# Kernel optimization log

Measured on AMD Instinct MI355X. Metric: run time of the kernel, lower is better.

The kernel has to match this reference:

```python
import jax, jax.numpy as jnp
import numpy as np

LN_EPS = 1e-5

def _layernorm(x, g, b):
    mu = jnp.mean(x, axis=-1, keepdims=True)
    var = jnp.var(x, axis=-1, keepdims=True)
    return (x - mu) / jnp.sqrt(var + LN_EPS) * g + b

def setup_inputs() -> dict:
    key = jax.random.key(0)
    ks = jax.random.split(key, 12)
    N, D_WSI, D_OMIC, D, DH = 50000, 1024, 1577, 256, 128
    def rn(k, shape, s=0.02):
        return jax.random.normal(k, shape, jnp.float32) * s
    return {
        'wsi': jax.random.normal(ks[0], (N, D_WSI), jnp.float32),
        'x_omic': jax.random.normal(ks[1], (D_OMIC,), jnp.float32),
        # SNNOmics: Linear(1577,256)+ELU, Linear(256,256)+ELU (AlphaDropout=eval identity)
        'W1': rn(ks[2], (D_OMIC, 256)), 'b1': jnp.zeros((256,), jnp.float32),
        'W2': rn(ks[3], (256, 256)), 'b2': jnp.zeros((256,), jnp.float32),
        # wsi projection Linear(1024,256)
        'Wp': rn(ks[4], (D_WSI, D)), 'bp': jnp.zeros((D,), jnp.float32),
        # MMAttentionLayer pre-norm (dim=256)
        'ln1_g': jnp.ones((D,), jnp.float32), 'ln1_b': jnp.zeros((D,), jnp.float32),
        # to_qkv: Linear(256, 3*heads*dim_head) = Linear(256, 384), no bias (heads=1, dim_head=128)
        'Wqkv': rn(ks[5], (D, 3 * DH)),
        # FeedForward(dim=128, mult=1): LN + Linear(128,128)+GELU+Linear(128,128) (no residual)
        'ln2_g': jnp.ones((DH,), jnp.float32), 'ln2_b': jnp.zeros((DH,), jnp.float32),
        'Wf1': rn(ks[6], (DH, DH)), 'bf1': jnp.zeros((DH,), jnp.float32),
        'Wf2': rn(ks[7], (DH, DH)), 'bf2': jnp.zeros((DH,), jnp.float32),
        # final LayerNorm(128)
        'ln3_g': jnp.ones((DH,), jnp.float32), 'ln3_b': jnp.zeros((DH,), jnp.float32),
        # to_logits: Linear(256,64)+ReLU+Linear(64,4)
        'Wl1': rn(ks[8], (2 * DH, 64)), 'bl1': jnp.zeros((64,), jnp.float32),
        'Wl2': rn(ks[9], (64, 4)), 'bl2': jnp.zeros((4,), jnp.float32),
    }

def reference(wsi, x_omic, W1, b1, W2, b2, Wp, bp, ln1_g, ln1_b, Wqkv,
              ln2_g, ln2_b, Wf1, bf1, Wf2, bf2, ln3_g, ln3_b, Wl1, bl1, Wl2, bl2):
    M = 1            # num_pathways
    DH = 128         # dim_head (heads=1)
    scale = DH ** -0.5
    # SNN omics encoder -> one pathway token [1, 256]
    h = jax.nn.elu(x_omic @ W1 + b1)
    h = jax.nn.elu(h @ W2 + b2)
    h_omic = h[None, :]                              # [1, 256]
    # WSI projection -> histology tokens [N, 256]
    wsi_embed = wsi @ Wp + bp                        # [N, 256]
    tokens = jnp.concatenate([h_omic, wsi_embed], axis=0)   # [1+N, 256]
    # MMAttentionLayer: pre-norm then asymmetric pathway/histology attention
    xn = _layernorm(tokens, ln1_g, ln1_b)
    qkv = xn @ Wqkv                                  # [1+N, 384]
    q, k, v = jnp.split(qkv, 3, axis=-1)             # each [1+N, 128]
    q = q * scale
    q_p, q_h = q[:M], q[M:]                          # [1,128], [N,128]
    k_p, k_h = k[:M], k[M:]
    # cross attention: histology -> pathways (rows of length M=1)
    cross_attn_hist = q_h @ k_p.T                    # [N, 1]
    cross_attn_hist = jax.nn.softmax(cross_attn_hist, axis=-1)
    # pathway row attends to [pathways | histology]
    attn_p = q_p @ k_p.T                             # [1, 1]
    cross_attn_p = q_p @ k_h.T                       # [1, N]
    attn_ph = jax.nn.softmax(jnp.concatenate([attn_p, cross_attn_p], axis=-1), axis=-1)  # [1, 1+N]
    out_p = attn_ph @ v                              # [1, 128]
    out_h = cross_attn_hist @ v[:M]                  # [N, 128]
    out = jnp.concatenate([out_p, out_h], axis=0)    # [1+N, 128] (residual=False: no conv)
    # FeedForward (no residual add in original) + LayerNorm
    mm = _layernorm(out, ln2_g, ln2_b)
    mm = jax.nn.gelu(mm @ Wf1 + bf1, approximate=False) @ Wf2 + bf2
    mm = _layernorm(mm, ln3_g, ln3_b)                # [1+N, 128]
    paths_embed = jnp.mean(mm[:M], axis=0)           # [128]
    wsi_embed_post = jnp.mean(mm[M:], axis=0)        # [128]
    embedding = jnp.concatenate([paths_embed, wsi_embed_post])[None, :]  # [1, 256]
    logits = jax.nn.relu(embedding @ Wl1 + bl1) @ Wl2 + bl2              # [1, 4]
    prob = jax.nn.softmax(logits, axis=-1)
    return logits, prob
```

## Files before the change

### kernel.cpp

```cpp
#include <hip/hip_runtime.h>
#include <hip/hip_bf16.h>
#include <math.h>

#define LN_EPS 1e-5f

typedef unsigned short ushortT;
typedef short bf16x8 __attribute__((ext_vector_type(8)));
typedef float f32x4 __attribute__((ext_vector_type(4)));

#define WS_QP   0
#define WS_V0   128
#define WS_S0   256
#define WS_H1P  512
#define WS_PART 4608
#define PART_STRIDE 260
#define PART_M 256
#define PART_L 257
#define WS_Z    107000
#define WS_GP   109000
#define GP_STRIDE 260
#define NCOMB   32
#define WS_WPT  131072

__device__ __forceinline__ float elu1(float x){ return x > 0.f ? x : expm1f(x); }
__device__ __forceinline__ unsigned pk2(float lo, float hi){
  union { __hip_bfloat162 h; unsigned u; } cv;
  cv.h = __float22bfloat162_rn(make_float2(lo, hi));
  return cv.u;
}
__device__ __forceinline__ void dma16(const void* g, void* l) {
  __builtin_amdgcn_global_load_lds(
      (const __attribute__((address_space(1))) unsigned int*)g,
      (__attribute__((address_space(3))) unsigned int*)l, 16, 0, 0);
}
template<int N> __device__ __forceinline__ void vwait() {
  asm volatile("s_waitcnt vmcnt(%0)" :: "i"(N) : "memory");
}
__device__ __forceinline__ void lwait0() {
  asm volatile("s_waitcnt lgkmcnt(0)" ::: "memory");
}
__device__ __forceinline__ void sbar()   { __builtin_amdgcn_s_barrier(); }
__device__ __forceinline__ void schedb() { __builtin_amdgcn_sched_barrier(0); }

__global__ __launch_bounds__(256) void k_setup(
    const float* __restrict__ Wp,
    const float* __restrict__ x, const float* __restrict__ W1, int d_omic,
    ushortT* __restrict__ wpt, float* __restrict__ ws)
{
  int bb = blockIdx.x, t = threadIdx.x;
  if (bb < 32) {
    int kc = bb, m = t, sw = (m >> 1) & 3;
    #pragma unroll
    for (int c = 0; c < 4; ++c) {
      float v[8];
      #pragma unroll
      for (int e = 0; e < 8; ++e) v[e] = Wp[(size_t)(kc * 32 + c * 8 + e) * 256 + m];
      uint4 w = make_uint4(pk2(v[0], v[1]), pk2(v[2], v[3]), pk2(v[4], v[5]), pk2(v[6], v[7]));
      *(uint4*)&wpt[kc * 8192 + m * 32 + ((c ^ sw) * 8)] = w;
    }
  } else {
    int g = bb - 32;
    int i0 = g * 99, i1 = min(i0 + 99, d_omic);
    __shared__ float xs[112];
    for (int i = i0 + t; i < i1; i += 256) xs[i - i0] = x[i];
    __syncthreads();
    float s = 0.f;
    for (int i = i0; i < i1; i++) s = fmaf(xs[i - i0], W1[(size_t)i * 256 + t], s);
    ws[WS_H1P + g * 256 + t] = s;
  }
}

__global__ __launch_bounds__(256) void k_omic(
    const float* __restrict__ b1,
    const float* __restrict__ W2, const float* __restrict__ b2,
    const float* __restrict__ Wqkv,
    const float* __restrict__ ln1_g, const float* __restrict__ ln1_b,
    float* __restrict__ ws)
{
  __shared__ float h1[256];
  __shared__ float xn0[256];
  __shared__ float qs[128], ks[128];
  __shared__ float red[8];
  int tid = threadIdx.x, lane = tid & 63, wave = tid >> 6;

  float s = b1[tid];
  for (int g = 0; g < 16; g++) s += ws[WS_H1P + g * 256 + tid];
  h1[tid] = elu1(s);
  __syncthreads();

  s = b2[tid];
  for (int i = 0; i < 256; i++) s = fmaf(h1[i], W2[i * 256 + tid], s);
  float t0 = elu1(s);

  float ps = t0, pq = t0 * t0;
  for (int m = 1; m < 64; m <<= 1) { ps += __shfl_xor(ps, m); pq += __shfl_xor(pq, m); }
  if (lane == 0) { red[wave] = ps; red[4 + wave] = pq; }
  __syncthreads();
  float mu = (red[0] + red[1] + red[2] + red[3]) * (1.f / 256.f);
  float var = (red[4] + red[5] + red[6] + red[7]) * (1.f / 256.f) - mu * mu;
  float xn = (t0 - mu) * rsqrtf(var + LN_EPS) * ln1_g[tid] + ln1_b[tid];
  xn0[tid] = xn;
  __syncthreads();

  float a = 0.f;
  for (int j = 0; j < 256; j++) a = fmaf(xn0[j], Wqkv[j * 384 + tid], a);
  if (tid < 128) { float q = a * 0.088388347648318447f; qs[tid] = q; ws[WS_QP + tid] = q; }
  else           { ks[tid - 128] = a; }
  if (tid < 128) {
    float av = 0.f;
    for (int j = 0; j < 256; j++) av = fmaf(xn0[j], Wqkv[j * 384 + 256 + tid], av);
    ws[WS_V0 + tid] = av;
  }
  __syncthreads();
  float p = (tid < 128) ? qs[tid] * ks[tid] : 0.f;
  for (int m = 1; m < 64; m <<= 1) p += __shfl_xor(p, m);
  if (lane == 0) red[wave] = p;
  __syncthreads();
  if (tid == 0) ws[WS_S0] = red[0] + red[1] + red[2] + red[3];

  float zv = 0.f;
  #pragma unroll 4
  for (int d = 0; d < 128; d += 4) {
    float4 q4 = *(const float4*)&qs[d];
    const float* wr_ = &Wqkv[tid * 384 + 128 + d];
    zv = fmaf(q4.x, wr_[0], zv);
    zv = fmaf(q4.y, wr_[1], zv);
    zv = fmaf(q4.z, wr_[2], zv);
    zv = fmaf(q4.w, wr_[3], zv);
  }
  ws[WS_Z + tid] = zv;
}

__global__ __launch_bounds__(512, 4) void k_main(
    const float* __restrict__ wsi, int N,
    const ushortT* __restrict__ wpt,
    const float* __restrict__ bp,
    const float* __restrict__ ln1_g, const float* __restrict__ ln1_b,
    float* __restrict__ ws)
{
  __shared__ __align__(16) char U[81920];

  const int tid = threadIdx.x;
  const int lane = tid & 63, wv = tid >> 6;
  const int l15 = lane & 15, lh = lane >> 4;
  const int cg = wv & 3, rg = wv >> 2;
  const int b = blockIdx.x, r0 = b * 128;

  int wsiSrc[2];
  #pragma unroll
  for (int i = 0; i < 2; ++i) {
    int rowL = 16 * wv + 8 * i + (lane >> 3);
    int gr = r0 + rowL; gr = (gr < N) ? gr : (N - 1);
    wsiSrc[i] = gr * 1024 + (((lane & 7) ^ (lane >> 3)) << 2);
  }
  int wptSrc[2];
  #pragma unroll
  for (int j = 0; j < 2; ++j) wptSrc[j] = (32 * wv + 16 * j) * 32 + lane * 8;

  const unsigned afslot = (unsigned)((lh ^ ((l15 >> 1) & 3)) << 4);
  const unsigned bs0 = (unsigned)(((2 * lh)     ^ (l15 & 7)) << 4);
  const unsigned bs1 = (unsigned)(((2 * lh + 1) ^ (l15 & 7)) << 4);

  const f32x4 z4i = {0.f, 0.f, 0.f, 0.f};
  f32x4 acc[4][4];
  #pragma unroll
  for (int mt = 0; mt < 4; ++mt)
    #pragma unroll
    for (int nt = 0; nt < 4; ++nt) acc[mt][nt] = z4i;

  auto stageWsi = [&](int kc, int slot) {
    char* ds = U + slot * 16384 + wv * 2048;
    #pragma unroll
    for (int i = 0; i < 2; ++i) dma16(wsi + wsiSrc[i] + kc * 32, ds + i * 1024);
  };
  auto stageWpt = [&](int kc, int slot) {
    char* dw = U + 49152 + slot * 16384 + wv * 2048;
    #pragma unroll
    for (int j = 0; j < 2; ++j) dma16(wpt + wptSrc[j] + kc * 8192, dw + j * 1024);
  };

  stageWsi(0, 0); stageWpt(0, 0);
  stageWsi(1, 1); stageWpt(1, 1);
  stageWsi(2, 2);
  for (int s = 0; s < 32; ++s) {
    if (s < 30) vwait<6>(); else if (s == 30) vwait<4>(); else vwait<0>();
    sbar(); schedb();
    {
      const char* Ws = U + (s % 3) * 16384;
      const char* Wf = U + 49152 + (s & 1) * 16384;
      bf16x8 af[4], bfr[4];
      #pragma unroll
      for (int mt = 0; mt < 4; ++mt)
        af[mt] = *(const bf16x8*)(Wf + (64 * cg + 16 * mt + l15) * 64 + afslot);
      #pragma unroll
      for (int nt = 0; nt < 4; ++nt) {
        const char* p = Ws + (64 * rg + 16 * nt + l15) * 128;
        uint4 ua = *(const uint4*)(p + bs0);
        uint4 ub = *(const uint4*)(p + bs1);
        union { unsigned u[4]; bf16x8 v; } cv;
        cv.u[0] = pk2(__uint_as_float(ua.x), __uint_as_float(ua.y));
        cv.u[1] = pk2(__uint_as_float(ua.z), __uint_as_float(ua.w));
        cv.u[2] = pk2(__uint_as_float(ub.x), __uint_as_float(ub.y));
        cv.u[3] = pk2(__uint_as_float(ub.z), __uint_as_float(ub.w));
        bfr[nt] = cv.v;
      }
      #pragma unroll
      for (int mt = 0; mt < 4; ++mt)
        #pragma unroll
        for (int nt = 0; nt < 4; ++nt)
          acc[mt][nt] = __builtin_amdgcn_mfma_f32_16x16x32_bf16(af[mt], bfr[nt], acc[mt][nt], 0, 0, 0);
    }
    sbar(); schedb();
    if (s < 30) stageWpt(s + 2, s & 1);
    if (s < 29) stageWsi(s + 3, s % 3);
  }

  float* red = (float*)(U + 65536);
  float4 bp4[4], g4[4], b4[4];
  #pragma unroll
  for (int mt = 0; mt < 4; ++mt) {
    int m0 = 64 * cg + 16 * mt + 4 * lh;
    bp4[mt] = *(const float4*)&bp[m0];
    g4[mt]  = *(const float4*)&ln1_g[m0];
    b4[mt]  = *(const float4*)&ln1_b[m0];
  }
  float ps[4], pq[4];
  #pragma unroll
  for (int nt = 0; nt < 4; ++nt) { ps[nt] = 0.f; pq[nt] = 0.f; }
  #pragma unroll
  for (int mt = 0; mt < 4; ++mt) {
    const float bb4[4] = {bp4[mt].x, bp4[mt].y, bp4[mt].z, bp4[mt].w};
    #pragma unroll
    for (int nt = 0; nt < 4; ++nt)
      #pragma unroll
      for (int r = 0; r < 4; ++r) {
        float v = acc[mt][nt][r] + bb4[r];
        acc[mt][nt][r] = v;
        ps[nt] += v; pq[nt] += v * v;
      }
  }
  #pragma unroll
  for (int nt = 0; nt < 4; ++nt) {
    ps[nt] += __shfl_xor(ps[nt], 16); pq[nt] += __shfl_xor(pq[nt], 16);
    ps[nt] += __shfl_xor(ps[nt], 32); pq[nt] += __shfl_xor(pq[nt], 32);
  }
  if (lh == 0) {
    #pragma unroll
    for (int nt = 0; nt < 4; ++nt) {
      int row = 64 * rg + 16 * nt + l15;
      *(float2*)&red[row * 8 + cg * 2] = make_float2(ps[nt], pq[nt]);
    }
  }
  lwait0(); sbar(); schedb();
  float mu[4], rstd[4];
  #pragma unroll
  for (int nt = 0; nt < 4; ++nt) {
    int row = 64 * rg + 16 * nt + l15;
    float s_ = 0.f, q_ = 0.f;
    #pragma unroll
    for (int c = 0; c < 4; ++c) { s_ += red[row * 8 + c * 2]; q_ += red[row * 8 + c * 2 + 1]; }
    float m_ = s_ * (1.f / 256.f);
    float v_ = q_ * (1.f / 256.f) - m_ * m_;
    mu[nt] = m_; rstd[nt] = rsqrtf(v_ + LN_EPS);
  }

  #pragma unroll
  for (int mt = 0; mt < 4; ++mt)
    #pragma unroll
    for (int nt = 0; nt < 4; ++nt) {
      acc[mt][nt][0] = (acc[mt][nt][0] - mu[nt]) * rstd[nt] * g4[mt].x + b4[mt].x;
      acc[mt][nt][1] = (acc[mt][nt][1] - mu[nt]) * rstd[nt] * g4[mt].y + b4[mt].y;
      acc[mt][nt][2] = (acc[mt][nt][2] - mu[nt]) * rstd[nt] * g4[mt].z + b4[mt].z;
      acc[mt][nt][3] = (acc[mt][nt][3] - mu[nt]) * rstd[nt] * g4[mt].w + b4[mt].w;
    }

  float* sred = (float*)U;
  float* aux  = (float*)(U + 2048);
  float* wts  = (float*)(U + 2112);
  float* vred = (float*)(U + 3072);
  float* part = ws + WS_PART + (size_t)b * PART_STRIDE;

  {
    float4 zf[4];
    #pragma unroll
    for (int mt = 0; mt < 4; ++mt)
      zf[mt] = *(const float4*)&ws[WS_Z + 64 * cg + 16 * mt + 4 * lh];
    float sp[4];
    #pragma unroll
    for (int nt = 0; nt < 4; ++nt) {
      float s_ = 0.f;
      #pragma unroll
      for (int mt = 0; mt < 4; ++mt) {
        s_ = fmaf(zf[mt].x, acc[mt][nt][0], s_);
        s_ = fmaf(zf[mt].y, acc[mt][nt][1], s_);
        s_ = fmaf(zf[mt].z, acc[mt][nt][2], s_);
        s_ = fmaf(zf[mt].w, acc[mt][nt][3], s_);
      }
      sp[nt] = s_;
    }
    #pragma unroll
    for (int nt = 0; nt < 4; ++nt) {
      sp[nt] += __shfl_xor(sp[nt], 16);
      sp[nt] += __shfl_xor(sp[nt], 32);
    }
    if (lh == 0) {
      #pragma unroll
      for (int nt = 0; nt < 4; ++nt) sred[cg * 128 + 64 * rg + 16 * nt + l15] = sp[nt];
    }
  }
  lwait0(); sbar(); schedb();

  float sv = -INFINITY, ev = 0.f;
  if (tid < 128) {
    sv = sred[tid] + sred[128 + tid] + sred[256 + tid] + sred[384 + tid];
    if (r0 + tid >= N) sv = -INFINITY;
  }
  float mb = sv;
  #pragma unroll
  for (int m = 1; m < 64; m <<= 1) mb = fmaxf(mb, __shfl_xor(mb, m));
  if (tid < 128 && lane == 0) aux[tid >> 6] = mb;
  lwait0(); sbar(); schedb();
  float M2 = fmaxf(aux[0], aux[1]);
  if (tid < 128) { ev = (r0 + tid < N) ? expf(sv - M2) : 0.f; wts[tid] = ev; }
  float lsum = ev;
  #pragma unroll
  for (int m = 1; m < 64; m <<= 1) lsum += __shfl_xor(lsum, m);
  if (tid < 128 && lane == 0) aux[2 + (tid >> 6)] = lsum;
  lwait0(); sbar(); schedb();
  if (tid == 0) { part[PART_M] = M2; part[PART_L] = aux[2] + aux[3]; }

  {
    float wr[4];
    #pragma unroll
    for (int nt = 0; nt < 4; ++nt) wr[nt] = wts[64 * rg + 16 * nt + l15];
    #pragma unroll
    for (int mt = 0; mt < 4; ++mt) {
      float vs0 = 0.f, vs1 = 0.f, vs2 = 0.f, vs3 = 0.f;
      #pragma unroll
      for (int nt = 0; nt < 4; ++nt) {
        vs0 = fmaf(wr[nt], acc[mt][nt][0], vs0);
        vs1 = fmaf(wr[nt], acc[mt][nt][1], vs1);
        vs2 = fmaf(wr[nt], acc[mt][nt][2], vs2);
        vs3 = fmaf(wr[nt], acc[mt][nt][3], vs3);
      }
      #pragma unroll
      for (int m = 1; m < 16; m <<= 1) {
        vs0 += __shfl_xor(vs0, m); vs1 += __shfl_xor(vs1, m);
        vs2 += __shfl_xor(vs2, m); vs3 += __shfl_xor(vs3, m);
      }
      if (l15 == 0)
        *(float4*)&vred[256 * rg + 64 * cg + 16 * mt + 4 * lh] =
            make_float4(vs0, vs1, vs2, vs3);
    }
  }
  lwait0(); sbar(); schedb();
  if (tid < 256) part[tid] = vred[tid] + vred[256 + tid];
}

__global__ __launch_bounds__(256) void k_fin1(float* __restrict__ ws, int NB, int chunk)
{
  int g = blockIdx.x, col = threadIdx.x;
  int c0 = g * chunk, c1 = min(c0 + chunk, NB);
  const float* part = ws + WS_PART;
  float mg = -INFINITY;
  for (int bb = c0; bb < c1; ++bb)
    mg = fmaxf(mg, part[(size_t)bb * PART_STRIDE + PART_M]);
  float a = 0.f, lg = 0.f;
  for (int bb = c0; bb < c1; ++bb) {
    float w = expf(part[(size_t)bb * PART_STRIDE + PART_M] - mg);
    a  = fmaf(part[(size_t)bb * PART_STRIDE + col], w, a);
    lg = fmaf(part[(size_t)bb * PART_STRIDE + PART_L], w, lg);
  }
  ws[WS_GP + g * GP_STRIDE + col] = a;
  if (col == 0) {
    ws[WS_GP + g * GP_STRIDE + PART_M] = mg;
    ws[WS_GP + g * GP_STRIDE + PART_L] = lg;
  }
}

__global__ __launch_bounds__(256) void k_final(
    const float* __restrict__ ws, const float* __restrict__ Wqkv,
    const float* __restrict__ Wf1, const float* __restrict__ bf1,
    const float* __restrict__ Wf2, const float* __restrict__ bf2,
    const float* __restrict__ ln2_g, const float* __restrict__ ln2_b,
    const float* __restrict__ ln3_g, const float* __restrict__ ln3_b,
    const float* __restrict__ Wl1, const float* __restrict__ bl1,
    const float* __restrict__ Wl2, const float* __restrict__ bl2,
    float* __restrict__ out)
{
  __shared__ float rowb[2][128];
  __shared__ float mmb[2][128];
  __shared__ float red[8];
  __shared__ float emb[256];
  __shared__ float abuf[64];
  __shared__ float lbuf[4];
  __shared__ float wg[NCOMB];
  __shared__ float MLs[2];
  __shared__ float Ybuf[256];
  int tid = threadIdx.x, lane = tid & 63, wave = tid >> 6;
  float s0 = ws[WS_S0];

  if (tid == 0) {
    float M = s0;
    for (int g = 0; g < NCOMB; ++g) M = fmaxf(M, ws[WS_GP + g * GP_STRIDE + PART_M]);
    float L = expf(s0 - M);
    for (int g = 0; g < NCOMB; ++g)
      L = fmaf(ws[WS_GP + g * GP_STRIDE + PART_L], expf(ws[WS_GP + g * GP_STRIDE + PART_M] - M), L);
    MLs[0] = M; MLs[1] = L;
  }
  __syncthreads();
  float M = MLs[0], L = MLs[1];
  if (tid < NCOMB) wg[tid] = expf(ws[WS_GP + tid * GP_STRIDE + PART_M] - M);
  __syncthreads();

  {
    float y = 0.f;
    #pragma unroll
    for (int g = 0; g < NCOMB; ++g) y = fmaf(ws[WS_GP + g * GP_STRIDE + tid], wg[g], y);
    Ybuf[tid] = y;
  }
  __syncthreads();

  if (tid < 128) {
    float v0 = ws[WS_V0 + tid];
    float a = v0 * expf(s0 - M);
    for (int c = 0; c < 256; ++c)
      a = fmaf(Ybuf[c], Wqkv[c * 384 + 256 + tid], a);
    rowb[0][tid] = a / L;
    rowb[1][tid] = v0;
  }
  __syncthreads();

  int row = tid >> 7, k = tid & 127;
  float x = rowb[row][k];
  float ps = x, pq = x * x;
  for (int m = 1; m < 64; m <<= 1) { ps += __shfl_xor(ps, m); pq += __shfl_xor(pq, m); }
  __syncthreads();
  if (lane == 0) { red[wave] = ps; red[4 + wave] = pq; }
  __syncthreads();
  {
    float sum = red[row * 2] + red[row * 2 + 1];
    float sq  = red[4 + row * 2] + red[4 + row * 2 + 1];
    float mu = sum * (1.f / 128.f);
    float var = sq * (1.f / 128.f) - mu * mu;
    x = (x - mu) * rsqrtf(var + LN_EPS) * ln2_g[k] + ln2_b[k];
  }
  mmb[row][k] = x;
  __syncthreads();
  float t1 = bf1[k];
  for (int j = 0; j < 128; j++) t1 = fmaf(mmb[row][j], Wf1[j * 128 + k], t1);
  float gg = t1 * 0.5f * (1.f + erff(t1 * 0.70710678118654752f));
  __syncthreads();
  rowb[row][k] = gg;
  __syncthreads();
  float t2 = bf2[k];
  for (int j = 0; j < 128; j++) t2 = fmaf(rowb[row][j], Wf2[j * 128 + k], t2);
  ps = t2; pq = t2 * t2;
  for (int m = 1; m < 64; m <<= 1) { ps += __shfl_xor(ps, m); pq += __shfl_xor(pq, m); }
  __syncthreads();
  if (lane == 0) { red[wave] = ps; red[4 + wave] = pq; }
  __syncthreads();
  {
    float sum = red[row * 2] + red[row * 2 + 1];
    float sq  = red[4 + row * 2] + red[4 + row * 2 + 1];
    float mu = sum * (1.f / 128.f);
    float var = sq * (1.f / 128.f) - mu * mu;
    t2 = (t2 - mu) * rsqrtf(var + LN_EPS) * ln3_g[k] + ln3_b[k];
  }
  emb[row * 128 + k] = t2;
  __syncthreads();
  if (tid < 64) {
    float a = bl1[tid];
    for (int j = 0; j < 256; j++) a = fmaf(emb[j], Wl1[j * 64 + tid], a);
    abuf[tid] = fmaxf(a, 0.f);
  }
  __syncthreads();
  if (tid < 4) {
    float lg = bl2[tid];
    for (int j = 0; j < 64; j++) lg = fmaf(abuf[j], Wl2[j * 4 + tid], lg);
    lbuf[tid] = lg;
  }
  __syncthreads();
  if (tid < 4) {
    float m4 = fmaxf(fmaxf(lbuf[0], lbuf[1]), fmaxf(lbuf[2], lbuf[3]));
    float e0 = expf(lbuf[0] - m4), e1 = expf(lbuf[1] - m4);
    float e2 = expf(lbuf[2] - m4), e3 = expf(lbuf[3] - m4);
    float ssum = e0 + e1 + e2 + e3;
    out[tid] = lbuf[tid];
    out[4 + tid] = expf(lbuf[tid] - m4) / ssum;
  }
}

extern "C" void kernel_launch(void* const* d_in, const int* in_sizes, int n_in,
                              void* d_out, int out_size, void* d_ws, size_t ws_size,
                              hipStream_t stream) {
  const float* wsi    = (const float*)d_in[0];
  const float* x_omic = (const float*)d_in[1];
  const float* W1     = (const float*)d_in[2];
  const float* b1     = (const float*)d_in[3];
  const float* W2     = (const float*)d_in[4];
  const float* b2     = (const float*)d_in[5];
  const float* Wp     = (const float*)d_in[6];
  const float* bp     = (const float*)d_in[7];
  const float* ln1_g  = (const float*)d_in[8];
  const float* ln1_b  = (const float*)d_in[9];
  const float* Wqkv   = (const float*)d_in[10];
  const float* ln2_g  = (const float*)d_in[11];
  const float* ln2_b  = (const float*)d_in[12];
  const float* Wf1    = (const float*)d_in[13];
  const float* bf1    = (const float*)d_in[14];
  const float* Wf2    = (const float*)d_in[15];
  const float* bf2    = (const float*)d_in[16];
  const float* ln3_g  = (const float*)d_in[17];
  const float* ln3_b  = (const float*)d_in[18];
  const float* Wl1    = (const float*)d_in[19];
  const float* bl1    = (const float*)d_in[20];
  const float* Wl2    = (const float*)d_in[21];
  const float* bl2    = (const float*)d_in[22];
  float* ws   = (float*)d_ws;
  float* outp = (float*)d_out;
  ushortT* wpt = (ushortT*)(ws + WS_WPT);

  int N = in_sizes[0] / 1024;
  int d_omic = in_sizes[1];
  int NB = (N + 127) / 128;
  int chunk = (NB + NCOMB - 1) / NCOMB;

  k_setup<<<48, 256, 0, stream>>>(Wp, x_omic, W1, d_omic, wpt, ws);
  k_omic<<<1, 256, 0, stream>>>(b1, W2, b2, Wqkv, ln1_g, ln1_b, ws);
  k_main<<<NB, 512, 0, stream>>>(wsi, N, wpt, bp, ln1_g, ln1_b, ws);
  k_fin1<<<NCOMB, 256, 0, stream>>>(ws, NB, chunk);
  k_final<<<1, 256, 0, stream>>>(ws, Wqkv, Wf1, bf1, Wf2, bf2, ln2_g, ln2_b,
                                 ln3_g, ln3_b, Wl1, bl1, Wl2, bl2, outp);
}
```

Measured before the change: 141.7 us.

## Halve k_main row tile and load weight fragments directly from global

The main projection kernel now processes 64 wsi rows per block instead of 128, which doubles the block count. The bf16 weight tile is no longer staged through LDS; each wave loads its A fragments from global memory (L2) into registers, double-buffered across pairs of K slices. This cuts shared memory from 80KB to 24KB and raises the launch-bounds occupancy target. In exchange the weights are reused less per block, global/L2 weight traffic rises, and more partial results have to be combined, so the partial buffer is moved to a larger workspace offset.

```diff
diff --git a/kernel.cpp b/kernel.cpp
--- a/kernel.cpp
+++ b/kernel.cpp
@@ -12,15 +12,15 @@
 #define WS_V0   128
 #define WS_S0   256
 #define WS_H1P  512
-#define WS_PART 4608
-#define PART_STRIDE 260
-#define PART_M 256
-#define PART_L 257
 #define WS_Z    107000
 #define WS_GP   109000
 #define GP_STRIDE 260
 #define NCOMB   32
 #define WS_WPT  131072
+#define WS_PART 262144
+#define PART_STRIDE 260
+#define PART_M 256
+#define PART_L 257
 
 __device__ __forceinline__ float elu1(float x){ return x > 0.f ? x : expm1f(x); }
 __device__ __forceinline__ unsigned pk2(float lo, float hi){
@@ -131,91 +131,95 @@
   ws[WS_Z + tid] = zv;
 }
 
-__global__ __launch_bounds__(512, 4) void k_main(
+__global__ __launch_bounds__(512, 6) void k_main(
     const float* __restrict__ wsi, int N,
     const ushortT* __restrict__ wpt,
     const float* __restrict__ bp,
     const float* __restrict__ ln1_g, const float* __restrict__ ln1_b,
     float* __restrict__ ws)
 {
-  __shared__ __align__(16) char U[81920];
+  __shared__ __align__(16) char U[24576];
 
   const int tid = threadIdx.x;
   const int lane = tid & 63, wv = tid >> 6;
   const int l15 = lane & 15, lh = lane >> 4;
   const int cg = wv & 3, rg = wv >> 2;
-  const int b = blockIdx.x, r0 = b * 128;
-
-  int wsiSrc[2];
-  #pragma unroll
-  for (int i = 0; i < 2; ++i) {
-    int rowL = 16 * wv + 8 * i + (lane >> 3);
+  const int b = blockIdx.x, r0 = b * 64;
+
+  int wsiSrc;
+  {
+    int rowL = 8 * wv + (lane >> 3);
     int gr = r0 + rowL; gr = (gr < N) ? gr : (N - 1);
-    wsiSrc[i] = gr * 1024 + (((lane & 7) ^ (lane >> 3)) << 2);
-  }
-  int wptSrc[2];
-  #pragma unroll
-  for (int j = 0; j < 2; ++j) wptSrc[j] = (32 * wv + 16 * j) * 32 + lane * 8;
-
-  const unsigned afslot = (unsigned)((lh ^ ((l15 >> 1) & 3)) << 4);
+    wsiSrc = gr * 1024 + (((lane & 7) ^ (lane >> 3)) << 2);
+  }
+  int afBase[4];
+  #pragma unroll
+  for (int mt = 0; mt < 4; ++mt) {
+    int m = 64 * cg + 16 * mt + l15;
+    afBase[mt] = m * 32 + ((lh ^ ((m >> 1) & 3)) << 3);
+  }
+
   const unsigned bs0 = (unsigned)(((2 * lh)     ^ (l15 & 7)) << 4);
   const unsigned bs1 = (unsigned)(((2 * lh + 1) ^ (l15 & 7)) << 4);
 
   const f32x4 z4i = {0.f, 0.f, 0.f, 0.f};
-  f32x4 acc[4][4];
+  f32x4 acc[4][2];
   #pragma unroll
   for (int mt = 0; mt < 4; ++mt)
     #pragma unroll
-    for (int nt = 0; nt < 4; ++nt) acc[mt][nt] = z4i;
+    for (int nt = 0; nt < 2; ++nt) acc[mt][nt] = z4i;
 
   auto stageWsi = [&](int kc, int slot) {
-    char* ds = U + slot * 16384 + wv * 2048;
-    #pragma unroll
-    for (int i = 0; i < 2; ++i) dma16(wsi + wsiSrc[i] + kc * 32, ds + i * 1024);
+    dma16(wsi + wsiSrc + kc * 32, U + slot * 8192 + wv * 1024);
   };
-  auto stageWpt = [&](int kc, int slot) {
-    char* dw = U + 49152 + slot * 16384 + wv * 2048;
-    #pragma unroll
-    for (int j = 0; j < 2; ++j) dma16(wpt + wptSrc[j] + kc * 8192, dw + j * 1024);
+
+  bf16x8 afA[4], afB[4];
+  auto loadAf = [&](bf16x8* dst, int kc) {
+    #pragma unroll
+    for (int mt = 0; mt < 4; ++mt)
+      dst[mt] = *(const bf16x8*)(wpt + (kc * 8192 + afBase[mt]));
   };
-
-  stageWsi(0, 0); stageWpt(0, 0);
-  stageWsi(1, 1); stageWpt(1, 1);
-  stageWsi(2, 2);
-  for (int s = 0; s < 32; ++s) {
-    if (s < 30) vwait<6>(); else if (s == 30) vwait<4>(); else vwait<0>();
+  auto computeSlice = [&](int s, const bf16x8* af) {
+    const char* Ws = U + (s % 3) * 8192;
+    bf16x8 bfr[2];
+    #pragma unroll
+    for (int nt = 0; nt < 2; ++nt) {
+      const char* p = Ws + (32 * rg + 16 * nt + l15) * 128;
+      uint4 ua = *(const uint4*)(p + bs0);
+      uint4 ub = *(const uint4*)(p + bs1);
+      union { unsigned u[4]; bf16x8 v; } cv;
+      cv.u[0] = pk2(__uint_as_float(ua.x), __uint_as_float(ua.y));
+      cv.u[1] = pk2(__uint_as_float(ua.z), __uint_as_float(ua.w));
+      cv.u[2] = pk2(__uint_as_float(ub.x), __uint_as_float(ub.y));
+      cv.u[3] = pk2(__uint_as_float(ub.z), __uint_as_float(ub.w));
+      bfr[nt] = cv.v;
+    }
+    #pragma unroll
+    for (int mt = 0; mt < 4; ++mt)
+      #pragma unroll
+      for (int nt = 0; nt < 2; ++nt)
+        acc[mt][nt] = __builtin_amdgcn_mfma_f32_16x16x32_bf16(af[mt], bfr[nt], acc[mt][nt], 0, 0, 0);
+  };
+
+  stageWsi(0, 0); stageWsi(1, 1); stageWsi(2, 2);
+  loadAf(afA, 0);
+  #pragma unroll 1
+  for (int sp = 0; sp < 16; ++sp) {
+    int s0 = 2 * sp, s1 = 2 * sp + 1;
+    vwait<6>(); sbar(); schedb();
+    if (s0 < 31) loadAf(afB, s1);
+    computeSlice(s0, afA);
     sbar(); schedb();
-    {
-      const char* Ws = U + (s % 3) * 16384;
-      const char* Wf = U + 49152 + (s & 1) * 16384;
-      bf16x8 af[4], bfr[4];
-      #pragma unroll
-      for (int mt = 0; mt < 4; ++mt)
-        af[mt] = *(const bf16x8*)(Wf + (64 * cg + 16 * mt + l15) * 64 + afslot);
-      #pragma unroll
-      for (int nt = 0; nt < 4; ++nt) {
-        const char* p = Ws + (64 * rg + 16 * nt + l15) * 128;
-        uint4 ua = *(const uint4*)(p + bs0);
-        uint4 ub = *(const uint4*)(p + bs1);
-        union { unsigned u[4]; bf16x8 v; } cv;
-        cv.u[0] = pk2(__uint_as_float(ua.x), __uint_as_float(ua.y));
-        cv.u[1] = pk2(__uint_as_float(ua.z), __uint_as_float(ua.w));
-        cv.u[2] = pk2(__uint_as_float(ub.x), __uint_as_float(ub.y));
-        cv.u[3] = pk2(__uint_as_float(ub.z), __uint_as_float(ub.w));
-        bfr[nt] = cv.v;
-      }
-      #pragma unroll
-      for (int mt = 0; mt < 4; ++mt)
-        #pragma unroll
-        for (int nt = 0; nt < 4; ++nt)
-          acc[mt][nt] = __builtin_amdgcn_mfma_f32_16x16x32_bf16(af[mt], bfr[nt], acc[mt][nt], 0, 0, 0);
-    }
+    if (s0 < 29) stageWsi(s0 + 3, (s0 + 3) % 3);
+    vwait<6>(); sbar(); schedb();
+    if (s1 < 31) loadAf(afA, s1 + 1);
+    computeSlice(s1, afB);
     sbar(); schedb();
-    if (s < 30) stageWpt(s + 2, s & 1);
-    if (s < 29) stageWsi(s + 3, s % 3);
-  }
-
-  float* red = (float*)(U + 65536);
+    if (s1 < 29) stageWsi(s1 + 3, (s1 + 3) % 3);
+  }
+  vwait<0>();
+
+  float* red = (float*)(U + 16384);
   float4 bp4[4], g4[4], b4[4];
   #pragma unroll
   for (int mt = 0; mt < 4; ++mt) {
@@ -224,14 +228,14 @@
     g4[mt]  = *(const float4*)&ln1_g[m0];
     b4[mt]  = *(const float4*)&ln1_b[m0];
   }
-  float ps[4], pq[4];
-  #pragma unroll
-  for (int nt = 0; nt < 4; ++nt) { ps[nt] = 0.f; pq[nt] = 0.f; }
+  float ps[2], pq[2];
+  #pragma unroll
+  for (int nt = 0; nt < 2; ++nt) { ps[nt] = 0.f; pq[nt] = 0.f; }
   #pragma unroll
   for (int mt = 0; mt < 4; ++mt) {
     const float bb4[4] = {bp4[mt].x, bp4[mt].y, bp4[mt].z, bp4[mt].w};
     #pragma unroll
-    for (int nt = 0; nt < 4; ++nt)
+    for (int nt = 0; nt < 2; ++nt)
       #pragma unroll
       for (int r = 0; r < 4; ++r) {
         float v = acc[mt][nt][r] + bb4[r];
@@ -240,22 +244,22 @@
       }
   }
   #pragma unroll
-  for (int nt = 0; nt < 4; ++nt) {
+  for (int nt = 0; nt < 2; ++nt) {
     ps[nt] += __shfl_xor(ps[nt], 16); pq[nt] += __shfl_xor(pq[nt], 16);
     ps[nt] += __shfl_xor(ps[nt], 32); pq[nt] += __shfl_xor(pq[nt], 32);
   }
   if (lh == 0) {
     #pragma unroll
-    for (int nt = 0; nt < 4; ++nt) {
-      int row = 64 * rg + 16 * nt + l15;
+    for (int nt = 0; nt < 2; ++nt) {
+      int row = 32 * rg + 16 * nt + l15;
       *(float2*)&red[row * 8 + cg * 2] = make_float2(ps[nt], pq[nt]);
     }
   }
   lwait0(); sbar(); schedb();
-  float mu[4], rstd[4];
-  #pragma unroll
-  for (int nt = 0; nt < 4; ++nt) {
-    int row = 64 * rg + 16 * nt + l15;
+  float mu[2], rstd[2];
+  #pragma unroll
+  for (int nt = 0; nt < 2; ++nt) {
+    int row = 32 * rg + 16 * nt + l15;
     float s_ = 0.f, q_ = 0.f;
     #pragma unroll
     for (int c = 0; c < 4; ++c) { s_ += red[row * 8 + c * 2]; q_ += red[row * 8 + c * 2 + 1]; }
@@ -263,21 +267,21 @@
     float v_ = q_ * (1.f / 256.f) - m_ * m_;
     mu[nt] = m_; rstd[nt] = rsqrtf(v_ + LN_EPS);
   }
-
   #pragma unroll
   for (int mt = 0; mt < 4; ++mt)
     #pragma unroll
-    for (int nt = 0; nt < 4; ++nt) {
+    for (int nt = 0; nt < 2; ++nt) {
       acc[mt][nt][0] = (acc[mt][nt][0] - mu[nt]) * rstd[nt] * g4[mt].x + b4[mt].x;
       acc[mt][nt][1] = (acc[mt][nt][1] - mu[nt]) * rstd[nt] * g4[mt].y + b4[mt].y;
       acc[mt][nt][2] = (acc[mt][nt][2] - mu[nt]) * rstd[nt] * g4[mt].z + b4[mt].z;
       acc[mt][nt][3] = (acc[mt][nt][3] - mu[nt]) * rstd[nt] * g4[mt].w + b4[mt].w;
     }
+  sbar(); schedb();
 
   float* sred = (float*)U;
-  float* aux  = (float*)(U + 2048);
-  float* wts  = (float*)(U + 2112);
-  float* vred = (float*)(U + 3072);
+  float* aux  = (float*)(U + 1024);
+  float* wts  = (float*)(U + 1056);
+  float* vred = (float*)(U + 1344);
   float* part = ws + WS_PART + (size_t)b * PART_STRIDE;
 
   {
@@ -285,9 +289,9 @@
     #pragma unroll
     for (int mt = 0; mt < 4; ++mt)
       zf[mt] = *(const float4*)&ws[WS_Z + 64 * cg + 16 * mt + 4 * lh];
-    float sp[4];
-    #pragma unroll
-    for (int nt = 0; nt < 4; ++nt) {
+    float sp[2];
+    #pragma unroll
+    for (int nt = 0; nt < 2; ++nt) {
       float s_ = 0.f;
       #pragma unroll
       for (int mt = 0; mt < 4; ++mt) {
@@ -299,45 +303,41 @@
       sp[nt] = s_;
     }
     #pragma unroll
-    for (int nt = 0; nt < 4; ++nt) {
+    for (int nt = 0; nt < 2; ++nt) {
       sp[nt] += __shfl_xor(sp[nt], 16);
       sp[nt] += __shfl_xor(sp[nt], 32);
     }
     if (lh == 0) {
       #pragma unroll
-      for (int nt = 0; nt < 4; ++nt) sred[cg * 128 + 64 * rg + 16 * nt + l15] = sp[nt];
+      for (int nt = 0; nt < 2; ++nt) sred[cg * 64 + 32 * rg + 16 * nt + l15] = sp[nt];
     }
   }
   lwait0(); sbar(); schedb();
 
-  float sv = -INFINITY, ev = 0.f;
-  if (tid < 128) {
-    sv = sred[tid] + sred[128 + tid] + sred[256 + tid] + sred[384 + tid];
+  if (tid < 64) {
+    float sv = sred[tid] + sred[64 + tid] + sred[128 + tid] + sred[192 + tid];
     if (r0 + tid >= N) sv = -INFINITY;
-  }
-  float mb = sv;
-  #pragma unroll
-  for (int m = 1; m < 64; m <<= 1) mb = fmaxf(mb, __shfl_xor(mb, m));
-  if (tid < 128 && lane == 0) aux[tid >> 6] = mb;
+    float mb = sv;
+    #pragma unroll
+    for (int m = 1; m < 64; m <<= 1) mb = fmaxf(mb, __shfl_xor(mb, m));
+    float ev = (r0 + tid < N) ? expf(sv - mb) : 0.f;
+    float lsum = ev;
+    #pragma unroll
+    for (int m = 1; m < 64; m <<= 1) lsum += __shfl_xor(lsum, m);
+    wts[tid] = ev;
+    if (tid == 0) { part[PART_M] = mb; part[PART_L] = lsum; }
+  }
   lwait0(); sbar(); schedb();
-  float M2 = fmaxf(aux[0], aux[1]);
-  if (tid < 128) { ev = (r0 + tid < N) ? expf(sv - M2) : 0.f; wts[tid] = ev; }
-  float lsum = ev;
-  #pragma unroll
-  for (int m = 1; m < 64; m <<= 1) lsum += __shfl_xor(lsum, m);
-  if (tid < 128 && lane == 0) aux[2 + (tid >> 6)] = lsum;
-  lwait0(); sbar(); schedb();
-  if (tid == 0) { part[PART_M] = M2; part[PART_L] = aux[2] + aux[3]; }
 
   {
-    float wr[4];
-    #pragma unroll
-    for (int nt = 0; nt < 4; ++nt) wr[nt] = wts[64 * rg + 16 * nt + l15];
+    float wr[2];
+    #pragma unroll
+    for (int nt = 0; nt < 2; ++nt) wr[nt] = wts[32 * rg + 16 * nt + l15];
     #pragma unroll
     for (int mt = 0; mt < 4; ++mt) {
       float vs0 = 0.f, vs1 = 0.f, vs2 = 0.f, vs3 = 0.f;
       #pragma unroll
-      for (int nt = 0; nt < 4; ++nt) {
+      for (int nt = 0; nt < 2; ++nt) {
         vs0 = fmaf(wr[nt], acc[mt][nt][0], vs0);
         vs1 = fmaf(wr[nt], acc[mt][nt][1], vs1);
         vs2 = fmaf(wr[nt], acc[mt][nt][2], vs2);
@@ -523,7 +523,7 @@
 
   int N = in_sizes[0] / 1024;
   int d_omic = in_sizes[1];
-  int NB = (N + 127) / 128;
+  int NB = (N + 63) / 64;
   int chunk = (NB + NCOMB - 1) / NCOMB;
 
   k_setup<<<48, 256, 0, stream>>>(Wp, x_omic, W1, d_omic, wpt, ws);
```

New measurement: 242.7 us. 1.71x slower.
